# Optimization experiments

Measured on AMD Instinct MI355X. Metric: run time of the kernel, lower is better.

Reference implementation:

```python
import jax, jax.numpy as jnp
import numpy as np

V, D, H, F, L, B, T = 32000, 512, 8, 2048, 4, 4, 1024
DK = D // H
S = 0.02  # init scale


def setup_inputs() -> dict:
    key = jax.random.key(0)
    ks = jax.random.split(key, 10)
    inp = {
        'x': jax.random.randint(ks[0], (B, T), 0, V),
        'embed': jax.random.normal(ks[1], (V, D), jnp.float32) * S,
        'Wq': jax.random.normal(ks[2], (L, D, D), jnp.float32) * S,
        'bq': jnp.zeros((L, D), jnp.float32),
        'Wk': jax.random.normal(ks[3], (L, D, D), jnp.float32) * S,
        'bk': jnp.zeros((L, D), jnp.float32),
        'Wv': jax.random.normal(ks[4], (L, D, D), jnp.float32) * S,
        'bv': jnp.zeros((L, D), jnp.float32),
        'Wo': jax.random.normal(ks[5], (L, D, D), jnp.float32) * S,
        'bo': jnp.zeros((L, D), jnp.float32),
        'ln1_s': jnp.ones((L, D), jnp.float32),
        'ln1_b': jnp.zeros((L, D), jnp.float32),
        'W1': jax.random.normal(ks[6], (L, D, F), jnp.float32) * S,
        'b1': jnp.zeros((L, F), jnp.float32),
        'W2': jax.random.normal(ks[7], (L, F, D), jnp.float32) * S,
        'b2': jnp.zeros((L, D), jnp.float32),
        'ln2_s': jnp.ones((L, D), jnp.float32),
        'ln2_b': jnp.zeros((L, D), jnp.float32),
        'lnf_s': jnp.ones((D,), jnp.float32),
        'lnf_b': jnp.zeros((D,), jnp.float32),
        'Wl': jax.random.normal(ks[8], (D, V), jnp.float32) * S,
        'bl': jnp.zeros((V,), jnp.float32),
    }
    return inp


def _layernorm(x, s, b, eps=1e-5):
    m = jnp.mean(x, axis=-1, keepdims=True)
    v = jnp.mean(jnp.square(x - m), axis=-1, keepdims=True)
    return (x - m) * jax.lax.rsqrt(v + eps) * s + b


def _forward(x, embed, Wq, bq, Wk, bk, Wv, bv, Wo, bo, ln1_s, ln1_b,
             W1, b1, W2, b2, ln2_s, ln2_b, lnf_s, lnf_b, Wl, bl):
    Bb, Tt = x.shape
    emb = embed.at[0].set(0.0)  # padding_idx = 0
    h = emb[x]  # [B,T,D]
    # sinusoidal positional encoding
    pos = jnp.arange(Tt, dtype=jnp.float32)[:, None]
    div = jnp.exp(jnp.arange(0, D, 2, dtype=jnp.float32) * (-np.log(10000.0) / D))
    pe = jnp.zeros((Tt, D), jnp.float32)
    pe = pe.at[:, 0::2].set(jnp.sin(pos * div)).at[:, 1::2].set(jnp.cos(pos * div))
    h = h + pe[None]
    # additive causal mask: 0 on/below diag, -inf above
    causal = jnp.triu(jnp.full((Tt, Tt), -jnp.inf, jnp.float32), 1)
    scale = 1.0 / np.sqrt(DK)
    for l in range(L):
        q = (h @ Wq[l] + bq[l]).reshape(Bb, Tt, H, DK)
        k = (h @ Wk[l] + bk[l]).reshape(Bb, Tt, H, DK)
        v = (h @ Wv[l] + bv[l]).reshape(Bb, Tt, H, DK)
        scores = jnp.einsum('bqhd,bkhd->bhqk', q, k) * scale + causal
        attn = jax.nn.softmax(scores, axis=-1)  # dropout=0 -> identity
        o = jnp.einsum('bhqk,bkhd->bqhd', attn, v).reshape(Bb, Tt, D)
        o = o @ Wo[l] + bo[l]
        h = _layernorm(h + o, ln1_s[l], ln1_b[l])
        ff = jax.nn.gelu(h @ W1[l] + b1[l], approximate=False) @ W2[l] + b2[l]
        h = _layernorm(h + ff, ln2_s[l], ln2_b[l])
    h = _layernorm(h, lnf_s, lnf_b)
    return h @ Wl + bl  # [B,T,V] logits


def reference(x, embed, Wq, bq, Wk, bk, Wv, bv, Wo, bo, ln1_s, ln1_b,
              W1, b1, W2, b2, ln2_s, ln2_b, lnf_s, lnf_b, Wl, bl):
    return _forward(x, embed, Wq, bq, Wk, bk, Wv, bv, Wo, bo, ln1_s, ln1_b,
                    W1, b1, W2, b2, ln2_s, ln2_b, lnf_s, lnf_b, Wl, bl)
```

## Files before the change

kernel.cpp:

```cpp
#include <hip/hip_runtime.h>
#include <math.h>

#define Mtot 4096
#define Dd   512
#define Hh   8
#define DKk  64
#define TT   1024
#define Ff   2048
#define Ll   4
#define Vv   32000

typedef __attribute__((ext_vector_type(8))) short bf16x8;
typedef __attribute__((ext_vector_type(4))) float f32x4;
typedef unsigned short u16;

__device__ __forceinline__ u16 f2b(float f) {
    union { float f; unsigned u; } x; x.f = f;
    unsigned r = x.u + 0x7fffu + ((x.u >> 16) & 1u);
    return (u16)(r >> 16);
}

typedef const __attribute__((address_space(1))) unsigned int* gp_t;
typedef __attribute__((address_space(3))) unsigned int* lp_t;
#define GLOAD_LDS16(g, l) __builtin_amdgcn_global_load_lds((gp_t)(const void*)(g), (lp_t)(void*)(l), 16, 0, 0)
#define VMCNT0 asm volatile("s_waitcnt vmcnt(0)" ::: "memory")

#define SWZ(row, c)  ((c) ^ (((row) & 7) << 3))
#define VSWZ(d, c)   ((c) ^ ((((d) ^ ((d) >> 3)) & 7) << 3))

__global__ __launch_bounds__(256) void embed_pe_kernel(const int* __restrict__ x,
                                                       const float* __restrict__ embed,
                                                       float* __restrict__ h,
                                                       u16* __restrict__ hb) {
    int idx = blockIdx.x * 256 + threadIdx.x;
    int d  = idx & (Dd - 1);
    int bt = idx >> 9;
    int t  = bt & (TT - 1);
    int tok = x[bt];
    float val = (tok == 0) ? 0.0f : embed[(size_t)tok * Dd + d];
    int de = d & ~1;
    float ang = (float)t * expf((float)de * (-9.210340371976184f / (float)Dd));
    val += (d & 1) ? cosf(ang) : sinf(ang);
    h[idx] = val;
    hb[idx] = f2b(val);
}

__global__ __launch_bounds__(256) void transpose_all(const float* __restrict__ Wq, const float* __restrict__ Wk,
                                                     const float* __restrict__ Wv, const float* __restrict__ Wo,
                                                     const float* __restrict__ W1, const float* __restrict__ W2,
                                                     const float* __restrict__ Wl,
                                                     u16* __restrict__ WqkvT, u16* __restrict__ WoT,
                                                     u16* __restrict__ W1T, u16* __restrict__ W2T,
                                                     u16* __restrict__ WlT) {
    __shared__ float t[32][33];
    int id = blockIdx.x;
    const float* src; u16* dst; int K, N, tx, ty;
    if (id < 12288) {
        int l = id / 3072, r = id - l * 3072;
        if (r < 768) {
            int which = r >> 8, t2 = r & 255;
            src = (which == 0 ? Wq : which == 1 ? Wk : Wv) + (size_t)l * 262144;
            dst = WqkvT + (size_t)l * 786432 + (size_t)which * 262144;
            K = 512; N = 512; ty = t2 >> 4; tx = t2 & 15;
        } else if (r < 1024) {
            int t2 = r - 768;
            src = Wo + (size_t)l * 262144; dst = WoT + (size_t)l * 262144;
            K = 512; N = 512; ty = t2 >> 4; tx = t2 & 15;
        } else if (r < 2048) {
            int t2 = r - 1024;
            src = W1 + (size_t)l * 1048576; dst = W1T + (size_t)l * 1048576;
            K = 512; N = 2048; ty = t2 >> 6; tx = t2 & 63;
        } else {
            int t2 = r - 2048;
            src = W2 + (size_t)l * 1048576; dst = W2T + (size_t)l * 1048576;
            K = 2048; N = 512; ty = t2 >> 4; tx = t2 & 15;
        }
    } else {
        int t2 = id - 12288;
        src = Wl; dst = WlT; K = 512; N = 32000;
        ty = t2 / 1000; tx = t2 - ty * 1000;
    }
    int n0 = tx * 32, k0 = ty * 32;
    int tid = threadIdx.x, c = tid & 31, rr = tid >> 5;
    #pragma unroll
    for (int i = 0; i < 4; i++)
        t[rr + i * 8][c] = src[(size_t)(k0 + rr + i * 8) * N + n0 + c];
    __syncthreads();
    #pragma unroll
    for (int i = 0; i < 4; i++)
        dst[(size_t)(n0 + rr + i * 8) * K + k0 + c] = f2b(t[c][rr + i * 8]);
}

__global__ __launch_bounds__(256) void biaspack_kernel(const float* __restrict__ bq,
                                                       const float* __restrict__ bk,
                                                       const float* __restrict__ bv,
                                                       float* __restrict__ bqkv) {
    int idx = blockIdx.x * 256 + threadIdx.x;
    int l = idx / 1536, j = idx - l * 1536;
    float v = (j < 512) ? bq[l * 512 + j] : (j < 1024) ? bk[l * 512 + j - 512] : bv[l * 512 + j - 1024];
    bqkv[idx] = v;
}

template<int ACT, int OUTB>
__global__ __launch_bounds__(512, 4) void mfma_gemm(const u16* __restrict__ A,
                                                    const u16* __restrict__ BT,
                                                    const float* __restrict__ bias,
                                                    float* __restrict__ outF,
                                                    u16* __restrict__ outB,
                                                    int M, int N, int K, int kbase, int klen, int gx) {
    __shared__ __align__(16) u16 As[2][128 * 32];
    __shared__ __align__(16) u16 Bs[2][128 * 32];
    int tid = threadIdx.x;
    int lane = tid & 63, w = tid >> 6;
    int nwg = gridDim.x, flat = blockIdx.x;
    int wg = (flat & 7) * (nwg >> 3) + (flat >> 3);
    int bm = wg / gx, bn = wg - bm * gx;
    int wr = w >> 2, wc = w & 3;
    int fr = lane & 15, fq = lane >> 4;

    int srow = tid >> 2, scol = (tid & 3) * 8;
    const u16* Ab = A  + (size_t)(bm * 128 + srow) * K + kbase + scol;
    const u16* Bb = BT + (size_t)(bn * 128 + srow) * K + kbase + scol;

    f32x4 acc[4][2] = {};
    int nk = klen >> 5;

    GLOAD_LDS16(Ab, &As[0][w * 512]);
    GLOAD_LDS16(Bb, &Bs[0][w * 512]);
    VMCNT0;
    __builtin_amdgcn_s_barrier();

    int cur = 0;
    for (int kt = 0; kt < nk; kt++) {
        if (kt + 1 < nk) {
            GLOAD_LDS16(Ab + (kt + 1) * 32, &As[cur ^ 1][w * 512]);
            GLOAD_LDS16(Bb + (kt + 1) * 32, &Bs[cur ^ 1][w * 512]);
        }
        bf16x8 a[4], b[2];
        #pragma unroll
        for (int m = 0; m < 4; m++) a[m] = *(const bf16x8*)&As[cur][(wr * 64 + m * 16 + fr) * 32 + fq * 8];
        #pragma unroll
        for (int n = 0; n < 2; n++) b[n] = *(const bf16x8*)&Bs[cur][(wc * 32 + n * 16 + fr) * 32 + fq * 8];
        __builtin_amdgcn_s_setprio(1);
        #pragma unroll
        for (int m = 0; m < 4; m++)
            #pragma unroll
            for (int n = 0; n < 2; n++)
                acc[m][n] = __builtin_amdgcn_mfma_f32_16x16x32_bf16(a[m], b[n], acc[m][n], 0, 0, 0);
        __builtin_amdgcn_s_setprio(0);
        __builtin_amdgcn_sched_barrier(0);
        VMCNT0;
        __builtin_amdgcn_s_barrier();
        cur ^= 1;
    }

    #pragma unroll
    for (int m = 0; m < 4; m++) {
        #pragma unroll
        for (int n = 0; n < 2; n++) {
            int col = bn * 128 + wc * 32 + n * 16 + fr;
            float bs = bias ? bias[col] : 0.0f;
            #pragma unroll
            for (int r = 0; r < 4; r++) {
                int row = bm * 128 + wr * 64 + m * 16 + fq * 4 + r;
                float v = acc[m][n][r] + bs;
                if (ACT == 1) v = 0.5f * v * (1.0f + erff(v * 0.7071067811865475f));
                if (OUTB) outB[(size_t)row * N + col] = f2b(v);
                else      outF[(size_t)row * N + col] = v;
            }
        }
    }
}

__global__ __launch_bounds__(256) void attn_mfma(const u16* __restrict__ qkv,
                                                 u16* __restrict__ ob) {
    int qt = (int)gridDim.x - 1 - (int)blockIdx.x;
    int hh = blockIdx.y, b = blockIdx.z;
    __shared__ __align__(16) u16 Qs[64 * 64];
    __shared__ __align__(16) u16 Ks[64 * 64];
    __shared__ __align__(16) u16 Vt[64 * 64];
    __shared__ __align__(16) u16 Ps[4][16 * 64];
    int tid = threadIdx.x;
    int lane = tid & 63, w = tid >> 6;
    int fr = lane & 15, fq = lane >> 4;
    int q0 = qt * 64;

    {
        int r = tid >> 2, c0 = (tid & 3) * 16;
        const u16* src = qkv + ((size_t)(b * TT + q0 + r)) * 1536 + hh * 64 + c0;
        bf16x8 v0 = *(const bf16x8*)src;
        bf16x8 v1 = *(const bf16x8*)(src + 8);
        *(bf16x8*)&Qs[r * 64 + SWZ(r, c0)]     = v0;
        *(bf16x8*)&Qs[r * 64 + SWZ(r, c0 + 8)] = v1;
    }
    __syncthreads();
    bf16x8 aq0 = *(const bf16x8*)&Qs[(w * 16 + fr) * 64 + SWZ(w * 16 + fr, fq * 8)];
    bf16x8 aq1 = *(const bf16x8*)&Qs[(w * 16 + fr) * 64 + SWZ(w * 16 + fr, 32 + fq * 8)];

    f32x4 oa[4] = {};
    float mreg[4], lreg[4];
    #pragma unroll
    for (int i = 0; i < 4; i++) { mreg[i] = -1e30f; lreg[i] = 0.0f; }

    for (int kt = 0; kt <= qt; kt++) {
        __syncthreads();
        {
            int r = tid >> 2, c0 = (tid & 3) * 16;
            const u16* srcK = qkv + ((size_t)(b * TT + kt * 64 + r)) * 1536 + 512 + hh * 64 + c0;
            bf16x8 k0v = *(const bf16x8*)srcK;
            bf16x8 k1v = *(const bf16x8*)(srcK + 8);
            *(bf16x8*)&Ks[r * 64 + SWZ(r, c0)]     = k0v;
            *(bf16x8*)&Ks[r * 64 + SWZ(r, c0 + 8)] = k1v;
            const u16* srcV = srcK + 512;
            bf16x8 vv0 = *(const bf16x8*)srcV;
            bf16x8 vv1 = *(const bf16x8*)(srcV + 8);
            #pragma unroll
            for (int j = 0; j < 8; j++) {
                int d0 = c0 + j, d1 = c0 + 8 + j;
                Vt[d0 * 64 + VSWZ(d0, r)] = (u16)vv0[j];
                Vt[d1 * 64 + VSWZ(d1, r)] = (u16)vv1[j];
            }
        }
        __syncthreads();

        f32x4 sa[4] = {};
        __builtin_amdgcn_s_setprio(1);
        #pragma unroll
        for (int nt = 0; nt < 4; nt++) {
            int krow = nt * 16 + fr;
            bf16x8 b0 = *(const bf16x8*)&Ks[krow * 64 + SWZ(krow, fq * 8)];
            bf16x8 b1 = *(const bf16x8*)&Ks[krow * 64 + SWZ(krow, 32 + fq * 8)];
            sa[nt] = __builtin_amdgcn_mfma_f32_16x16x32_bf16(aq0, b0, sa[nt], 0, 0, 0);
            sa[nt] = __builtin_amdgcn_mfma_f32_16x16x32_bf16(aq1, b1, sa[nt], 0, 0, 0);
        }
        __builtin_amdgcn_s_setprio(0);

        float p[4][4];
        int qg = w * 16 + fq * 4;
        bool diag = (kt == qt);
        #pragma unroll
        for (int nt = 0; nt < 4; nt++)
            #pragma unroll
            for (int i = 0; i < 4; i++) {
                float s = sa[nt][i] * 0.125f;
                if (diag && (nt * 16 + fr > qg + i)) s = -1e30f;
                p[nt][i] = s;
            }

        float mnew[4], fscale[4];
        #pragma unroll
        for (int i = 0; i < 4; i++) {
            float v = fmaxf(fmaxf(p[0][i], p[1][i]), fmaxf(p[2][i], p[3][i]));
            v = fmaxf(v, __shfl_xor(v, 1));
            v = fmaxf(v, __shfl_xor(v, 2));
            v = fmaxf(v, __shfl_xor(v, 4));
            v = fmaxf(v, __shfl_xor(v, 8));
            mnew[i] = fmaxf(mreg[i], v);
            fscale[i] = __expf(mreg[i] - mnew[i]);
            mreg[i] = mnew[i];
        }
        #pragma unroll
        for (int i = 0; i < 4; i++) {
            float sum = 0.f;
            #pragma unroll
            for (int nt = 0; nt < 4; nt++) {
                float e = __expf(p[nt][i] - mnew[i]);
                p[nt][i] = e;
                sum += e;
            }
            sum += __shfl_xor(sum, 1);
            sum += __shfl_xor(sum, 2);
            sum += __shfl_xor(sum, 4);
            sum += __shfl_xor(sum, 8);
            lreg[i] = lreg[i] * fscale[i] + sum;
        }
        #pragma unroll
        for (int nn = 0; nn < 4; nn++)
            #pragma unroll
            for (int i = 0; i < 4; i++)
                oa[nn][i] *= fscale[i];

        u16* ps = &Ps[w][0];
        #pragma unroll
        for (int nt = 0; nt < 4; nt++)
            #pragma unroll
            for (int i = 0; i < 4; i++) {
                int row = fq * 4 + i, col = nt * 16 + fr;
                ps[row * 64 + SWZ(row, col)] = f2b(p[nt][i]);
            }
        bf16x8 pa0 = *(const bf16x8*)&ps[fr * 64 + SWZ(fr, fq * 8)];
        bf16x8 pa1 = *(const bf16x8*)&ps[fr * 64 + SWZ(fr, 32 + fq * 8)];
        __builtin_amdgcn_s_setprio(1);
        #pragma unroll
        for (int nn = 0; nn < 4; nn++) {
            int drow = nn * 16 + fr;
            bf16x8 vb0 = *(const bf16x8*)&Vt[drow * 64 + VSWZ(drow, fq * 8)];
            bf16x8 vb1 = *(const bf16x8*)&Vt[drow * 64 + VSWZ(drow, 32 + fq * 8)];
            oa[nn] = __builtin_amdgcn_mfma_f32_16x16x32_bf16(pa0, vb0, oa[nn], 0, 0, 0);
            oa[nn] = __builtin_amdgcn_mfma_f32_16x16x32_bf16(pa1, vb1, oa[nn], 0, 0, 0);
        }
        __builtin_amdgcn_s_setprio(0);
    }

    #pragma unroll
    for (int i = 0; i < 4; i++) {
        float inv = 1.0f / lreg[i];
        size_t row = (size_t)(b * TT + q0 + w * 16 + fq * 4 + i) * Dd + hh * 64;
        #pragma unroll
        for (int nn = 0; nn < 4; nn++)
            ob[row + nn * 16 + fr] = f2b(oa[nn][i] * inv);
    }
}

__global__ __launch_bounds__(256) void ln_kernel(float* __restrict__ h,
                                                 const float* __restrict__ d1,
                                                 const float* __restrict__ d2,
                                                 const float* __restrict__ gs,
                                                 const float* __restrict__ gb,
                                                 u16* __restrict__ hb) {
    int w = threadIdx.x >> 6, lane = threadIdx.x & 63;
    int row = (blockIdx.x << 2) + w;
    size_t base = (size_t)row * Dd + lane * 8;
    f32x4 v0 = *(const f32x4*)&h[base];
    f32x4 v1 = *(const f32x4*)&h[base + 4];
    if (d1) { v0 += *(const f32x4*)&d1[base]; v1 += *(const f32x4*)&d1[base + 4]; }
    if (d2) { v0 += *(const f32x4*)&d2[base]; v1 += *(const f32x4*)&d2[base + 4]; }
    float s = v0[0] + v0[1] + v0[2] + v0[3] + v1[0] + v1[1] + v1[2] + v1[3];
    #pragma unroll
    for (int st = 1; st < 64; st <<= 1) s += __shfl_xor(s, st);
    float m = s * (1.0f / Dd);
    float q = 0.f;
    #pragma unroll
    for (int j = 0; j < 4; j++) { float a = v0[j] - m, b = v1[j] - m; q += a * a + b * b; }
    #pragma unroll
    for (int st = 1; st < 64; st <<= 1) q += __shfl_xor(q, st);
    float r = rsqrtf(q * (1.0f / Dd) + 1e-5f);
    f32x4 g0 = *(const f32x4*)&gs[lane * 8],     g1 = *(const f32x4*)&gs[lane * 8 + 4];
    f32x4 c0 = *(const f32x4*)&gb[lane * 8],     c1 = *(const f32x4*)&gb[lane * 8 + 4];
    f32x4 y0, y1;
    bf16x8 yb;
    #pragma unroll
    for (int j = 0; j < 4; j++) {
        y0[j] = (v0[j] - m) * r * g0[j] + c0[j];
        y1[j] = (v1[j] - m) * r * g1[j] + c1[j];
        yb[j]     = (short)f2b(y0[j]);
        yb[j + 4] = (short)f2b(y1[j]);
    }
    *(f32x4*)&h[base]     = y0;
    *(f32x4*)&h[base + 4] = y1;
    *(bf16x8*)&hb[base]   = yb;
}

extern "C" void kernel_launch(void* const* d_in, const int* in_sizes, int n_in,
                              void* d_out, int out_size, void* d_ws, size_t ws_size,
                              hipStream_t stream) {
    const int*   x     = (const int*)  d_in[0];
    const float* embed = (const float*)d_in[1];
    const float* Wq    = (const float*)d_in[2];
    const float* bq    = (const float*)d_in[3];
    const float* Wk    = (const float*)d_in[4];
    const float* bk    = (const float*)d_in[5];
    const float* Wv    = (const float*)d_in[6];
    const float* bv    = (const float*)d_in[7];
    const float* Wo    = (const float*)d_in[8];
    const float* bo    = (const float*)d_in[9];
    const float* ln1_s = (const float*)d_in[10];
    const float* ln1_b = (const float*)d_in[11];
    const float* W1    = (const float*)d_in[12];
    const float* b1    = (const float*)d_in[13];
    const float* W2    = (const float*)d_in[14];
    const float* b2    = (const float*)d_in[15];
    const float* ln2_s = (const float*)d_in[16];
    const float* ln2_b = (const float*)d_in[17];
    const float* lnf_s = (const float*)d_in[18];
    const float* lnf_b = (const float*)d_in[19];
    const float* Wl    = (const float*)d_in[20];
    const float* bl    = (const float*)d_in[21];

    char* wp = (char*)d_ws;
    float* h    = (float*)wp;  wp += (size_t)Mtot * Dd * 4;
    float* pb   = (float*)wp;  wp += (size_t)Mtot * Dd * 4;
    float* pb2  = (float*)wp;  wp += (size_t)Mtot * Dd * 4;
    u16*   hb   = (u16*)wp;    wp += (size_t)Mtot * Dd * 2;
    u16*   qkvb = (u16*)wp;    wp += (size_t)Mtot * 1536 * 2;
    u16*   obb  = (u16*)wp;    wp += (size_t)Mtot * Dd * 2;
    u16*   fbb  = (u16*)wp;    wp += (size_t)Mtot * Ff * 2;
    u16*   WlT  = (u16*)wp;    wp += (size_t)Vv * Dd * 2;
    float* bqkv = (float*)wp;  wp += (size_t)Ll * 1536 * 4;

    char* op = (char*)d_out;
    u16* WqkvT = (u16*)op;  op += (size_t)Ll * 1536 * Dd * 2;
    u16* WoT   = (u16*)op;  op += (size_t)Ll * Dd * Dd * 2;
    u16* W1T   = (u16*)op;  op += (size_t)Ll * Ff * Dd * 2;
    u16* W2T   = (u16*)op;  op += (size_t)Ll * Dd * Ff * 2;

    transpose_all<<<28288, 256, 0, stream>>>(Wq, Wk, Wv, Wo, W1, W2, Wl, WqkvT, WoT, W1T, W2T, WlT);
    biaspack_kernel<<<24, 256, 0, stream>>>(bq, bk, bv, bqkv);
    embed_pe_kernel<<<(Mtot * Dd) / 256, 256, 0, stream>>>(x, embed, h, hb);

    for (int l = 0; l < Ll; l++) {
        mfma_gemm<0, 1><<<(1536 / 128) * (Mtot / 128), 512, 0, stream>>>(
            hb, WqkvT + (size_t)l * 1536 * Dd, bqkv + l * 1536, nullptr, qkvb,
            Mtot, 1536, Dd, 0, Dd, 1536 / 128);
        attn_mfma<<<dim3(TT / 64, Hh, 4), 256, 0, stream>>>(qkvb, obb);
        mfma_gemm<0, 0><<<(Dd / 128) * (Mtot / 128), 512, 0, stream>>>(
            obb, WoT + (size_t)l * Dd * Dd, bo + l * Dd, pb, nullptr,
            Mtot, Dd, Dd, 0, Dd / 2, Dd / 128);
        mfma_gemm<0, 0><<<(Dd / 128) * (Mtot / 128), 512, 0, stream>>>(
            obb, WoT + (size_t)l * Dd * Dd, nullptr, pb2, nullptr,
            Mtot, Dd, Dd, Dd / 2, Dd / 2, Dd / 128);
        ln_kernel<<<Mtot / 4, 256, 0, stream>>>(h, pb, pb2, ln1_s + l * Dd, ln1_b + l * Dd, hb);
        mfma_gemm<1, 1><<<(Ff / 128) * (Mtot / 128), 512, 0, stream>>>(
            hb, W1T + (size_t)l * Ff * Dd, b1 + l * Ff, nullptr, fbb,
            Mtot, Ff, Dd, 0, Dd, Ff / 128);
        mfma_gemm<0, 0><<<(Dd / 128) * (Mtot / 128), 512, 0, stream>>>(
            fbb, W2T + (size_t)l * Dd * Ff, b2 + l * Dd, pb, nullptr,
            Mtot, Dd, Ff, 0, Ff / 2, Dd / 128);
        mfma_gemm<0, 0><<<(Dd / 128) * (Mtot / 128), 512, 0, stream>>>(
            fbb, W2T + (size_t)l * Dd * Ff, nullptr, pb2, nullptr,
            Mtot, Dd, Ff, Ff / 2, Ff / 2, Dd / 128);
        ln_kernel<<<Mtot / 4, 256, 0, stream>>>(h, pb, pb2, ln2_s + l * Dd, ln2_b + l * Dd, hb);
    }

    ln_kernel<<<Mtot / 4, 256, 0, stream>>>(h, nullptr, nullptr, lnf_s, lnf_b, hb);
    mfma_gemm<0, 0><<<(Vv / 128) * (Mtot / 128), 512, 0, stream>>>(
        hb, WlT, bl, (float*)d_out, nullptr, Mtot, Vv, Dd, 0, Dd, Vv / 128);
}
```

Measured before the change: 903.1 us.

## Retile GEMM to 4-wave BK64 double-buffered pipeline, write V transposed, prefetch attention tiles

The GEMM now uses 256 threads, each wave computing a 64x64 subtile with K=64 stages. Global-to-LDS loads are XOR-swizzled and issued two stages ahead, with partial vmcnt waits. The split-K Wo/W2 launches and their second partial buffer are removed. The QKV GEMM writes V directly in a transposed per-head layout, which removes the scalar LDS transpose inside attention, and attention register-prefetches the next K/V tile while computing the current one. The price is more registers per thread and fewer blocks for the D=512 output GEMMs now that split-K is gone.

Result: faster. 828.5 us (-8.3%).

```diff
diff --git a/kernel.cpp b/kernel.cpp
--- a/kernel.cpp
+++ b/kernel.cpp
@@ -23,10 +23,10 @@
 typedef const __attribute__((address_space(1))) unsigned int* gp_t;
 typedef __attribute__((address_space(3))) unsigned int* lp_t;
 #define GLOAD_LDS16(g, l) __builtin_amdgcn_global_load_lds((gp_t)(const void*)(g), (lp_t)(void*)(l), 16, 0, 0)
-#define VMCNT0 asm volatile("s_waitcnt vmcnt(0)" ::: "memory")
+#define SBAR  __builtin_amdgcn_s_barrier()
+#define SCHED0 __builtin_amdgcn_sched_barrier(0)
 
 #define SWZ(row, c)  ((c) ^ (((row) & 7) << 3))
-#define VSWZ(d, c)   ((c) ^ ((((d) ^ ((d) >> 3)) & 7) << 3))
 
 __global__ __launch_bounds__(256) void embed_pe_kernel(const int* __restrict__ x,
                                                        const float* __restrict__ embed,
@@ -101,97 +101,162 @@
     bqkv[idx] = v;
 }
 
-template<int ACT, int OUTB>
-__global__ __launch_bounds__(512, 4) void mfma_gemm(const u16* __restrict__ A,
+template<int ACT, int OUTB, int QKVMODE>
+__global__ __launch_bounds__(256, 2) void mfma_gemm(const u16* __restrict__ A,
                                                     const u16* __restrict__ BT,
                                                     const float* __restrict__ bias,
                                                     float* __restrict__ outF,
                                                     u16* __restrict__ outB,
-                                                    int M, int N, int K, int kbase, int klen, int gx) {
-    __shared__ __align__(16) u16 As[2][128 * 32];
-    __shared__ __align__(16) u16 Bs[2][128 * 32];
+                                                    u16* __restrict__ vtb,
+                                                    int M, int N, int K, int gx) {
+    __shared__ __align__(16) u16 As[2][128 * 64];
+    __shared__ __align__(16) u16 Bs[2][128 * 64];
     int tid = threadIdx.x;
     int lane = tid & 63, w = tid >> 6;
     int nwg = gridDim.x, flat = blockIdx.x;
     int wg = (flat & 7) * (nwg >> 3) + (flat >> 3);
     int bm = wg / gx, bn = wg - bm * gx;
-    int wr = w >> 2, wc = w & 3;
+    int wr = w >> 1, wc = w & 1;
     int fr = lane & 15, fq = lane >> 4;
 
-    int srow = tid >> 2, scol = (tid & 3) * 8;
-    const u16* Ab = A  + (size_t)(bm * 128 + srow) * K + kbase + scol;
-    const u16* Bb = BT + (size_t)(bn * 128 + srow) * K + kbase + scol;
-
-    f32x4 acc[4][2] = {};
-    int nk = klen >> 5;
-
-    GLOAD_LDS16(Ab, &As[0][w * 512]);
-    GLOAD_LDS16(Bb, &Bs[0][w * 512]);
-    VMCNT0;
-    __builtin_amdgcn_s_barrier();
+    int sr = lane >> 3, sc = lane & 7;
+    int scol = (sc ^ sr) * 8;
+    const u16* Ab = A  + (size_t)(bm * 128 + w * 32 + sr) * K + scol;
+    const u16* Bb = BT + (size_t)(bn * 128 + w * 32 + sr) * K + scol;
+    u16* lA = &As[0][0] + w * 2048;
+    u16* lB = &Bs[0][0] + w * 2048;
+
+    f32x4 acc[4][4] = {};
+    int nk = K >> 6;
+
+#define STAGE(buf, kt)                                                     \
+    {   int ko = (kt) * 64;                                                \
+        GLOAD_LDS16(Ab + ko,          lA + (buf) * (128 * 64));            \
+        GLOAD_LDS16(Ab + 8 * K + ko,  lA + (buf) * (128 * 64) + 512);      \
+        GLOAD_LDS16(Ab + 16 * K + ko, lA + (buf) * (128 * 64) + 1024);     \
+        GLOAD_LDS16(Ab + 24 * K + ko, lA + (buf) * (128 * 64) + 1536);     \
+        GLOAD_LDS16(Bb + ko,          lB + (buf) * (128 * 64));            \
+        GLOAD_LDS16(Bb + 8 * K + ko,  lB + (buf) * (128 * 64) + 512);      \
+        GLOAD_LDS16(Bb + 16 * K + ko, lB + (buf) * (128 * 64) + 1024);     \
+        GLOAD_LDS16(Bb + 24 * K + ko, lB + (buf) * (128 * 64) + 1536); }
+
+    STAGE(0, 0);
+    STAGE(1, 1);
 
     int cur = 0;
     for (int kt = 0; kt < nk; kt++) {
-        if (kt + 1 < nk) {
-            GLOAD_LDS16(Ab + (kt + 1) * 32, &As[cur ^ 1][w * 512]);
-            GLOAD_LDS16(Bb + (kt + 1) * 32, &Bs[cur ^ 1][w * 512]);
-        }
-        bf16x8 a[4], b[2];
-        #pragma unroll
-        for (int m = 0; m < 4; m++) a[m] = *(const bf16x8*)&As[cur][(wr * 64 + m * 16 + fr) * 32 + fq * 8];
-        #pragma unroll
-        for (int n = 0; n < 2; n++) b[n] = *(const bf16x8*)&Bs[cur][(wc * 32 + n * 16 + fr) * 32 + fq * 8];
+        if (kt + 1 < nk) { asm volatile("s_waitcnt vmcnt(8)" ::: "memory"); }
+        else             { asm volatile("s_waitcnt vmcnt(0)" ::: "memory"); }
+        SBAR;
+        SCHED0;
+        bf16x8 a[4][2], b[4][2];
+        #pragma unroll
+        for (int m = 0; m < 4; m++) {
+            int row = wr * 64 + m * 16 + fr;
+            a[m][0] = *(const bf16x8*)&As[cur][row * 64 + ((fq ^ (row & 7)) * 8)];
+            a[m][1] = *(const bf16x8*)&As[cur][row * 64 + (((fq + 4) ^ (row & 7)) * 8)];
+        }
+        #pragma unroll
+        for (int n = 0; n < 4; n++) {
+            int row = wc * 64 + n * 16 + fr;
+            b[n][0] = *(const bf16x8*)&Bs[cur][row * 64 + ((fq ^ (row & 7)) * 8)];
+            b[n][1] = *(const bf16x8*)&Bs[cur][row * 64 + (((fq + 4) ^ (row & 7)) * 8)];
+        }
         __builtin_amdgcn_s_setprio(1);
         #pragma unroll
         for (int m = 0; m < 4; m++)
             #pragma unroll
-            for (int n = 0; n < 2; n++)
-                acc[m][n] = __builtin_amdgcn_mfma_f32_16x16x32_bf16(a[m], b[n], acc[m][n], 0, 0, 0);
+            for (int n = 0; n < 4; n++) {
+                acc[m][n] = __builtin_amdgcn_mfma_f32_16x16x32_bf16(a[m][0], b[n][0], acc[m][n], 0, 0, 0);
+                acc[m][n] = __builtin_amdgcn_mfma_f32_16x16x32_bf16(a[m][1], b[n][1], acc[m][n], 0, 0, 0);
+            }
         __builtin_amdgcn_s_setprio(0);
-        __builtin_amdgcn_sched_barrier(0);
-        VMCNT0;
-        __builtin_amdgcn_s_barrier();
+        SCHED0;
+        SBAR;
+        SCHED0;
+        if (kt + 2 < nk) STAGE(cur, kt + 2);
         cur ^= 1;
     }
+#undef STAGE
 
     #pragma unroll
     for (int m = 0; m < 4; m++) {
         #pragma unroll
-        for (int n = 0; n < 2; n++) {
-            int col = bn * 128 + wc * 32 + n * 16 + fr;
+        for (int n = 0; n < 4; n++) {
+            int col = bn * 128 + wc * 64 + n * 16 + fr;
             float bs = bias ? bias[col] : 0.0f;
-            #pragma unroll
-            for (int r = 0; r < 4; r++) {
-                int row = bm * 128 + wr * 64 + m * 16 + fq * 4 + r;
-                float v = acc[m][n][r] + bs;
-                if (ACT == 1) v = 0.5f * v * (1.0f + erff(v * 0.7071067811865475f));
-                if (OUTB) outB[(size_t)row * N + col] = f2b(v);
-                else      outF[(size_t)row * N + col] = v;
+            if (QKVMODE && bn >= 8) {
+                int hh = (col - 1024) >> 6, d = (col - 1024) & 63;
+                #pragma unroll
+                for (int r = 0; r < 4; r++) {
+                    int row = bm * 128 + wr * 64 + m * 16 + fq * 4 + r;
+                    int bb = row >> 10, t = row & 1023;
+                    vtb[(((size_t)bb * Hh + hh) * 64 + d) * 1024 + t] = f2b(acc[m][n][r] + bs);
+                }
+            } else {
+                #pragma unroll
+                for (int r = 0; r < 4; r++) {
+                    int row = bm * 128 + wr * 64 + m * 16 + fq * 4 + r;
+                    float v = acc[m][n][r] + bs;
+                    if (ACT == 1) v = 0.5f * v * (1.0f + erff(v * 0.7071067811865475f));
+                    if (OUTB) outB[(size_t)row * N + col] = f2b(v);
+                    else      outF[(size_t)row * N + col] = v;
+                }
             }
         }
     }
 }
 
 __global__ __launch_bounds__(256) void attn_mfma(const u16* __restrict__ qkv,
+                                                 const u16* __restrict__ vtb,
                                                  u16* __restrict__ ob) {
     int qt = (int)gridDim.x - 1 - (int)blockIdx.x;
     int hh = blockIdx.y, b = blockIdx.z;
     __shared__ __align__(16) u16 Qs[64 * 64];
     __shared__ __align__(16) u16 Ks[64 * 64];
-    __shared__ __align__(16) u16 Vt[64 * 64];
+    __shared__ __align__(16) u16 Vs[64 * 64];
     __shared__ __align__(16) u16 Ps[4][16 * 64];
     int tid = threadIdx.x;
     int lane = tid & 63, w = tid >> 6;
     int fr = lane & 15, fq = lane >> 4;
     int q0 = qt * 64;
-
+    int sr = tid >> 2, sc0 = (tid & 3) * 16;
+
+    bf16x8 rk0, rk1, rv0, rv1;
+    bf16x8 sk0, sk1, sv0, sv1;
+
+    auto load_a = [&](int kt) {
+        const u16* srcK = qkv + ((size_t)(b * TT + kt * 64 + sr)) * 1536 + 512 + hh * 64 + sc0;
+        rk0 = *(const bf16x8*)srcK; rk1 = *(const bf16x8*)(srcK + 8);
+        const u16* srcV = vtb + (((size_t)(b * Hh + hh)) * 64 + sr) * 1024 + kt * 64 + sc0;
+        rv0 = *(const bf16x8*)srcV; rv1 = *(const bf16x8*)(srcV + 8);
+    };
+    auto load_b = [&](int kt) {
+        const u16* srcK = qkv + ((size_t)(b * TT + kt * 64 + sr)) * 1536 + 512 + hh * 64 + sc0;
+        sk0 = *(const bf16x8*)srcK; sk1 = *(const bf16x8*)(srcK + 8);
+        const u16* srcV = vtb + (((size_t)(b * Hh + hh)) * 64 + sr) * 1024 + kt * 64 + sc0;
+        sv0 = *(const bf16x8*)srcV; sv1 = *(const bf16x8*)(srcV + 8);
+    };
+    auto store_a = [&]() {
+        *(bf16x8*)&Ks[sr * 64 + SWZ(sr, sc0)]     = rk0;
+        *(bf16x8*)&Ks[sr * 64 + SWZ(sr, sc0 + 8)] = rk1;
+        *(bf16x8*)&Vs[sr * 64 + SWZ(sr, sc0)]     = rv0;
+        *(bf16x8*)&Vs[sr * 64 + SWZ(sr, sc0 + 8)] = rv1;
+    };
+    auto store_b = [&]() {
+        *(bf16x8*)&Ks[sr * 64 + SWZ(sr, sc0)]     = sk0;
+        *(bf16x8*)&Ks[sr * 64 + SWZ(sr, sc0 + 8)] = sk1;
+        *(bf16x8*)&Vs[sr * 64 + SWZ(sr, sc0)]     = sv0;
+        *(bf16x8*)&Vs[sr * 64 + SWZ(sr, sc0 + 8)] = sv1;
+    };
+
+    load_a(0);
     {
-        int r = tid >> 2, c0 = (tid & 3) * 16;
-        const u16* src = qkv + ((size_t)(b * TT + q0 + r)) * 1536 + hh * 64 + c0;
+        const u16* src = qkv + ((size_t)(b * TT + q0 + sr)) * 1536 + hh * 64 + sc0;
         bf16x8 v0 = *(const bf16x8*)src;
         bf16x8 v1 = *(const bf16x8*)(src + 8);
-        *(bf16x8*)&Qs[r * 64 + SWZ(r, c0)]     = v0;
-        *(bf16x8*)&Qs[r * 64 + SWZ(r, c0 + 8)] = v1;
+        *(bf16x8*)&Qs[sr * 64 + SWZ(sr, sc0)]     = v0;
+        *(bf16x8*)&Qs[sr * 64 + SWZ(sr, sc0 + 8)] = v1;
     }
     __syncthreads();
     bf16x8 aq0 = *(const bf16x8*)&Qs[(w * 16 + fr) * 64 + SWZ(w * 16 + fr, fq * 8)];
@@ -202,27 +267,7 @@
     #pragma unroll
     for (int i = 0; i < 4; i++) { mreg[i] = -1e30f; lreg[i] = 0.0f; }
 
-    for (int kt = 0; kt <= qt; kt++) {
-        __syncthreads();
-        {
-            int r = tid >> 2, c0 = (tid & 3) * 16;
-            const u16* srcK = qkv + ((size_t)(b * TT + kt * 64 + r)) * 1536 + 512 + hh * 64 + c0;
-            bf16x8 k0v = *(const bf16x8*)srcK;
-            bf16x8 k1v = *(const bf16x8*)(srcK + 8);
-            *(bf16x8*)&Ks[r * 64 + SWZ(r, c0)]     = k0v;
-            *(bf16x8*)&Ks[r * 64 + SWZ(r, c0 + 8)] = k1v;
-            const u16* srcV = srcK + 512;
-            bf16x8 vv0 = *(const bf16x8*)srcV;
-            bf16x8 vv1 = *(const bf16x8*)(srcV + 8);
-            #pragma unroll
-            for (int j = 0; j < 8; j++) {
-                int d0 = c0 + j, d1 = c0 + 8 + j;
-                Vt[d0 * 64 + VSWZ(d0, r)] = (u16)vv0[j];
-                Vt[d1 * 64 + VSWZ(d1, r)] = (u16)vv1[j];
-            }
-        }
-        __syncthreads();
-
+    auto compute_tile = [&](int kt) {
         f32x4 sa[4] = {};
         __builtin_amdgcn_s_setprio(1);
         #pragma unroll
@@ -294,12 +339,31 @@
         #pragma unroll
         for (int nn = 0; nn < 4; nn++) {
             int drow = nn * 16 + fr;
-            bf16x8 vb0 = *(const bf16x8*)&Vt[drow * 64 + VSWZ(drow, fq * 8)];
-            bf16x8 vb1 = *(const bf16x8*)&Vt[drow * 64 + VSWZ(drow, 32 + fq * 8)];
+            bf16x8 vb0 = *(const bf16x8*)&Vs[drow * 64 + SWZ(drow, fq * 8)];
+            bf16x8 vb1 = *(const bf16x8*)&Vs[drow * 64 + SWZ(drow, 32 + fq * 8)];
             oa[nn] = __builtin_amdgcn_mfma_f32_16x16x32_bf16(pa0, vb0, oa[nn], 0, 0, 0);
             oa[nn] = __builtin_amdgcn_mfma_f32_16x16x32_bf16(pa1, vb1, oa[nn], 0, 0, 0);
         }
         __builtin_amdgcn_s_setprio(0);
+    };
+
+    int kt = 0;
+    for (;;) {
+        SCHED0; SBAR;
+        store_a();
+        if (kt + 1 <= qt) load_b(kt + 1);
+        asm volatile("s_waitcnt lgkmcnt(0)" ::: "memory");
+        SBAR; SCHED0;
+        compute_tile(kt);
+        if (++kt > qt) break;
+
+        SCHED0; SBAR;
+        store_b();
+        if (kt + 1 <= qt) load_a(kt + 1);
+        asm volatile("s_waitcnt lgkmcnt(0)" ::: "memory");
+        SBAR; SCHED0;
+        compute_tile(kt);
+        if (++kt > qt) break;
     }
 
     #pragma unroll
@@ -314,7 +378,6 @@
 
 __global__ __launch_bounds__(256) void ln_kernel(float* __restrict__ h,
                                                  const float* __restrict__ d1,
-                                                 const float* __restrict__ d2,
                                                  const float* __restrict__ gs,
                                                  const float* __restrict__ gb,
                                                  u16* __restrict__ hb) {
@@ -324,7 +387,6 @@
     f32x4 v0 = *(const f32x4*)&h[base];
     f32x4 v1 = *(const f32x4*)&h[base + 4];
     if (d1) { v0 += *(const f32x4*)&d1[base]; v1 += *(const f32x4*)&d1[base + 4]; }
-    if (d2) { v0 += *(const f32x4*)&d2[base]; v1 += *(const f32x4*)&d2[base + 4]; }
     float s = v0[0] + v0[1] + v0[2] + v0[3] + v1[0] + v1[1] + v1[2] + v1[3];
     #pragma unroll
     for (int st = 1; st < 64; st <<= 1) s += __shfl_xor(s, st);
@@ -380,9 +442,9 @@
     char* wp = (char*)d_ws;
     float* h    = (float*)wp;  wp += (size_t)Mtot * Dd * 4;
     float* pb   = (float*)wp;  wp += (size_t)Mtot * Dd * 4;
-    float* pb2  = (float*)wp;  wp += (size_t)Mtot * Dd * 4;
     u16*   hb   = (u16*)wp;    wp += (size_t)Mtot * Dd * 2;
     u16*   qkvb = (u16*)wp;    wp += (size_t)Mtot * 1536 * 2;
+    u16*   vtb  = (u16*)wp;    wp += (size_t)Mtot * Dd * 2;
     u16*   obb  = (u16*)wp;    wp += (size_t)Mtot * Dd * 2;
     u16*   fbb  = (u16*)wp;    wp += (size_t)Mtot * Ff * 2;
     u16*   WlT  = (u16*)wp;    wp += (size_t)Vv * Dd * 2;
@@ -399,30 +461,24 @@
     embed_pe_kernel<<<(Mtot * Dd) / 256, 256, 0, stream>>>(x, embed, h, hb);
 
     for (int l = 0; l < Ll; l++) {
-        mfma_gemm<0, 1><<<(1536 / 128) * (Mtot / 128), 512, 0, stream>>>(
-            hb, WqkvT + (size_t)l * 1536 * Dd, bqkv + l * 1536, nullptr, qkvb,
-            Mtot, 1536, Dd, 0, Dd, 1536 / 128);
-        attn_mfma<<<dim3(TT / 64, Hh, 4), 256, 0, stream>>>(qkvb, obb);
-        mfma_gemm<0, 0><<<(Dd / 128) * (Mtot / 128), 512, 0, stream>>>(
-            obb, WoT + (size_t)l * Dd * Dd, bo + l * Dd, pb, nullptr,
-            Mtot, Dd, Dd, 0, Dd / 2, Dd / 128);
-        mfma_gemm<0, 0><<<(Dd / 128) * (Mtot / 128), 512, 0, stream>>>(
-            obb, WoT + (size_t)l * Dd * Dd, nullptr, pb2, nullptr,
-            Mtot, Dd, Dd, Dd / 2, Dd / 2, Dd / 128);
-        ln_kernel<<<Mtot / 4, 256, 0, stream>>>(h, pb, pb2, ln1_s + l * Dd, ln1_b + l * Dd, hb);
-        mfma_gemm<1, 1><<<(Ff / 128) * (Mtot / 128), 512, 0, stream>>>(
-            hb, W1T + (size_t)l * Ff * Dd, b1 + l * Ff, nullptr, fbb,
-            Mtot, Ff, Dd, 0, Dd, Ff / 128);
-        mfma_gemm<0, 0><<<(Dd / 128) * (Mtot / 128), 512, 0, stream>>>(
-            fbb, W2T + (size_t)l * Dd * Ff, b2 + l * Dd, pb, nullptr,
-            Mtot, Dd, Ff, 0, Ff / 2, Dd / 128);
-        mfma_gemm<0, 0><<<(Dd / 128) * (Mtot / 128), 512, 0, stream>>>(
-            fbb, W2T + (size_t)l * Dd * Ff, nullptr, pb2, nullptr,
-            Mtot, Dd, Ff, Ff / 2, Ff / 2, Dd / 128);
-        ln_kernel<<<Mtot / 4, 256, 0, stream>>>(h, pb, pb2, ln2_s + l * Dd, ln2_b + l * Dd, hb);
-    }
-
-    ln_kernel<<<Mtot / 4, 256, 0, stream>>>(h, nullptr, nullptr, lnf_s, lnf_b, hb);
-    mfma_gemm<0, 0><<<(Vv / 128) * (Mtot / 128), 512, 0, stream>>>(
-        hb, WlT, bl, (float*)d_out, nullptr, Mtot, Vv, Dd, 0, Dd, Vv / 128);
-}
+        mfma_gemm<0, 1, 1><<<(1536 / 128) * (Mtot / 128), 256, 0, stream>>>(
+            hb, WqkvT + (size_t)l * 1536 * Dd, bqkv + l * 1536, nullptr, qkvb, vtb,
+            Mtot, 1536, Dd, 1536 / 128);
+        attn_mfma<<<dim3(TT / 64, Hh, 4), 256, 0, stream>>>(qkvb, vtb, obb);
+        mfma_gemm<0, 0, 0><<<(Dd / 128) * (Mtot / 128), 256, 0, stream>>>(
+            obb, WoT + (size_t)l * Dd * Dd, bo + l * Dd, pb, nullptr, nullptr,
+            Mtot, Dd, Dd, Dd / 128);
+        ln_kernel<<<Mtot / 4, 256, 0, stream>>>(h, pb, ln1_s + l * Dd, ln1_b + l * Dd, hb);
+        mfma_gemm<1, 1, 0><<<(Ff / 128) * (Mtot / 128), 256, 0, stream>>>(
+            hb, W1T + (size_t)l * Ff * Dd, b1 + l * Ff, nullptr, fbb, nullptr,
+            Mtot, Ff, Dd, Ff / 128);
+        mfma_gemm<0, 0, 0><<<(Dd / 128) * (Mtot / 128), 256, 0, stream>>>(
+            fbb, W2T + (size_t)l * Dd * Ff, b2 + l * Dd, pb, nullptr, nullptr,
+            Mtot, Dd, Ff, Dd / 128);
+        ln_kernel<<<Mtot / 4, 256, 0, stream>>>(h, pb, ln2_s + l * Dd, ln2_b + l * Dd, hb);
+    }
+
+    ln_kernel<<<Mtot / 4, 256, 0, stream>>>(h, nullptr, lnf_s, lnf_b, hb);
+    mfma_gemm<0, 0, 0><<<(Vv / 128) * (Mtot / 128), 256, 0, stream>>>(
+        hb, WlT, bl, (float*)d_out, nullptr, nullptr, Mtot, Vv, Dd, Vv / 128);
+}
```
